# Performance work log

Measured on AMD Instinct MI355X. Metric: run time of the kernel, lower is better.

Reference implementation:

```python
import jax, jax.numpy as jnp
import numpy as np

N_NODES = 100000
D_IN = 128
D_OUT = 128
N_REL = 4
N_EDGES = 500000


def setup_inputs() -> dict:
    key = jax.random.key(0)
    k_x, k_e, k_w, k_b, k_ws, k_bs = jax.random.split(key, 6)
    x = jax.random.normal(k_x, (N_NODES, D_IN), dtype=jnp.float32)
    # edge_indices[r] = [2, E]: row 0 = source node ids, row 1 = target node ids
    edge_indices = jax.random.randint(k_e, (N_REL, 2, N_EDGES), 0, N_NODES, dtype=jnp.int32)
    scale = 1.0 / np.sqrt(D_IN)
    # per-relation Linear weights (out, in) and biases, like nn.Linear
    W = jax.random.uniform(k_w, (N_REL, D_OUT, D_IN), dtype=jnp.float32, minval=-scale, maxval=scale)
    b = jax.random.uniform(k_b, (N_REL, D_OUT), dtype=jnp.float32, minval=-scale, maxval=scale)
    W_sl = jax.random.uniform(k_ws, (D_OUT, D_IN), dtype=jnp.float32, minval=-scale, maxval=scale)
    b_sl = jax.random.uniform(k_bs, (D_OUT,), dtype=jnp.float32, minval=-scale, maxval=scale)
    return {"x": x, "edge_indices": edge_indices, "W": W, "b": b, "W_sl": W_sl, "b_sl": b_sl}


def reference(x, edge_indices, W, b, W_sl, b_sl):
    # gather source features per relation: [R, E, D_IN]
    src = edge_indices[:, 0]  # [R, E]
    tgt = edge_indices[:, 1]  # [R, E]
    xs = x[src]  # [R, E, D_IN]
    # per-relation linear (nn.Linear: x @ W.T + b): [R, E, D_OUT]
    msgs = jnp.einsum('red,rfd->ref', xs, W) + b[:, None, :]
    # scatter-add into per-relation node accumulators, then sum over relations
    agg = jax.vmap(lambda m, t: jax.ops.segment_sum(m, t, num_segments=N_NODES))(msgs, tgt)
    agg = agg.sum(axis=0)  # [N, D_OUT]
    # self loop
    agg = agg + x @ W_sl.T + b_sl
    return agg
```

## Files before the change

### kernel.cpp

```cpp
#include <hip/hip_runtime.h>
#include <hip/hip_bf16.h>

#define N_NODES 100000
#define D 128
#define N_REL 4
#define N_EDGES 500000
#define N_CNT (N_REL * N_NODES)
#define SCAN_CHUNK 1024
#define N_SCAN_BLK ((N_CNT + SCAN_CHUNK - 1) / SCAN_CHUNK)
#define SORT_MAX (N_REL * N_EDGES + 3 * N_CNT)

typedef __attribute__((ext_vector_type(8))) short bf16x8;
typedef __attribute__((ext_vector_type(4))) float f32x4;

__device__ __forceinline__ unsigned short f2bf(float f) {
    unsigned int u = __float_as_uint(f);
    u += 0x7fffu + ((u >> 16) & 1u);
    return (unsigned short)(u >> 16);
}

#define CVT_BLOCKS 6250
#define WB_BLOCKS 320
#define ZR_BLOCKS 1
#define HIST_BLOCKS 7813
__global__ __launch_bounds__(256) void prep_kernel(const float* __restrict__ x,
                                                   const int* __restrict__ ei,
                                                   const float* __restrict__ W,
                                                   const float* __restrict__ W_sl,
                                                   ushort* __restrict__ xbf,
                                                   ushort* __restrict__ WbT,
                                                   int* __restrict__ cnt) {
    const int b = blockIdx.x, tid = threadIdx.x;
    if (b < CVT_BLOCKS) {
        size_t t = (size_t)b * 256 + tid;
        float4 v0 = ((const float4*)x)[t * 2];
        float4 v1 = ((const float4*)x)[t * 2 + 1];
        int4 o;
        o.x = ((int)f2bf(v0.y) << 16) | f2bf(v0.x);
        o.y = ((int)f2bf(v0.w) << 16) | f2bf(v0.z);
        o.z = ((int)f2bf(v1.y) << 16) | f2bf(v1.x);
        o.w = ((int)f2bf(v1.w) << 16) | f2bf(v1.z);
        ((int4*)xbf)[t] = o;
    } else if (b < CVT_BLOCKS + WB_BLOCKS) {
        int t = (b - CVT_BLOCKS) * 256 + tid;
        int f = t / 640;
        int k = t - f * 640;
        float v;
        if (k < 512) {
            int r = k >> 7, d = k & 127;
            v = W[((size_t)r * 128 + f) * 128 + d];
        } else {
            v = W_sl[(size_t)f * 128 + (k - 512)];
        }
        WbT[t] = f2bf(v);
    } else if (b < CVT_BLOCKS + WB_BLOCKS + ZR_BLOCKS) {
        if (tid < 16) ((uint4*)(xbf + (size_t)N_NODES * D))[tid] = make_uint4(0, 0, 0, 0);
    } else {
        int t = (b - CVT_BLOCKS - WB_BLOCKS - ZR_BLOCKS) * 256 + tid;
        if (t >= N_REL * N_EDGES) return;
        int r = t / N_EDGES;
        int e = t - r * N_EDGES;
        int tgt = ei[(size_t)r * 2 * N_EDGES + N_EDGES + e];
        atomicAdd(&cnt[r * N_NODES + tgt], 1);
    }
}

__global__ __launch_bounds__(256) void scanA(const int* __restrict__ cnt,
                                             int* __restrict__ foff,
                                             int* __restrict__ partials) {
    __shared__ int ps[256];
    int b = blockIdx.x, t = threadIdx.x;
    int i0 = b * SCAN_CHUNK + t * 4;
    int v[4];
#pragma unroll
    for (int q = 0; q < 4; ++q) v[q] = (i0 + q < N_CNT) ? ((cnt[i0 + q] + 3) & ~3) : 0;
    int s = v[0] + v[1] + v[2] + v[3];
    ps[t] = s;
    __syncthreads();
    for (int d = 1; d < 256; d <<= 1) {
        int u = (t >= d) ? ps[t - d] : 0;
        __syncthreads();
        ps[t] += u;
        __syncthreads();
    }
    if (t == 255) partials[b] = ps[255];
    int run = (t == 0) ? 0 : ps[t - 1];
#pragma unroll
    for (int q = 0; q < 4; ++q) {
        if (i0 + q < N_CNT) foff[i0 + q] = run;
        run += v[q];
    }
}
__global__ __launch_bounds__(512) void scanB(int* __restrict__ partials,
                                             int* __restrict__ foff) {
    __shared__ int ps[512];
    int t = threadIdx.x;
    ps[t] = (t < N_SCAN_BLK) ? partials[t] : 0;
    __syncthreads();
    for (int d = 1; d < 512; d <<= 1) {
        int u = (t >= d) ? ps[t - d] : 0;
        __syncthreads();
        ps[t] += u;
        __syncthreads();
    }
    if (t < N_SCAN_BLK) partials[t] = (t == 0) ? 0 : ps[t - 1];
    if (t == N_SCAN_BLK - 1) foff[N_CNT] = ps[t];
}
__global__ __launch_bounds__(256) void scanC(int* __restrict__ foff,
                                             const int* __restrict__ partials,
                                             const int* __restrict__ cnt,
                                             int* __restrict__ cur0,
                                             int* __restrict__ sorted) {
    int i = blockIdx.x * 256 + threadIdx.x;
    if (i >= N_CNT) return;
    int base = foff[i] + partials[i >> 10];
    foff[i] = base;
    cur0[i] = 0;
    int c = cnt[i];
    int cp = (c + 3) & ~3;
    for (int j = c; j < cp; ++j) sorted[base + j] = N_NODES;
}

__global__ __launch_bounds__(256) void bucket_kernel(const int* __restrict__ ei,
                                                     const int* __restrict__ foff,
                                                     int* __restrict__ cur0,
                                                     int* __restrict__ sorted) {
    int t = blockIdx.x * 256 + threadIdx.x;
    if (t >= N_REL * N_EDGES) return;
    int r = t / N_EDGES;
    int e = t - r * N_EDGES;
    int src = ei[(size_t)r * 2 * N_EDGES + e];
    int tgt = ei[(size_t)r * 2 * N_EDGES + N_EDGES + e];
    int i = r * N_NODES + tgt;
    int pos = foff[i] + atomicAdd(&cur0[i], 1);
    sorted[pos] = src;
}

__global__ __launch_bounds__(256) void gather_kernel(const ushort* __restrict__ xbf,
                                                     const int* __restrict__ sorted,
                                                     const int* __restrict__ foff,
                                                     unsigned int* __restrict__ buf) {
    int wid = (blockIdx.x * 256 + threadIdx.x) >> 6;
    wid = __builtin_amdgcn_readfirstlane(wid);
    const int lane = threadIdx.x & 63;
    const int p0 = wid * 4;
    int f0 = foff[p0], f1 = foff[p0 + 1], f2 = foff[p0 + 2], f3 = foff[p0 + 3], f4 = foff[p0 + 4];
#pragma unroll
    for (int pi = 0; pi < 4; ++pi) {
        int gb = (pi == 0) ? f0 : (pi == 1) ? f1 : (pi == 2) ? f2 : f3;
        int ge = (pi == 0) ? f1 : (pi == 1) ? f2 : (pi == 2) ? f3 : f4;
        float ax = 0.f, ay = 0.f;
        for (int g = gb; g < ge; g += 4) {
            int4 s = *(const int4*)(sorted + g);
            unsigned int u0 = ((const unsigned int*)(xbf + ((size_t)s.x << 7)))[lane];
            unsigned int u1 = ((const unsigned int*)(xbf + ((size_t)s.y << 7)))[lane];
            unsigned int u2 = ((const unsigned int*)(xbf + ((size_t)s.z << 7)))[lane];
            unsigned int u3 = ((const unsigned int*)(xbf + ((size_t)s.w << 7)))[lane];
            ax += __uint_as_float(u0 << 16) + __uint_as_float(u1 << 16)
                + __uint_as_float(u2 << 16) + __uint_as_float(u3 << 16);
            ay += __uint_as_float(u0 & 0xffff0000u) + __uint_as_float(u1 & 0xffff0000u)
                + __uint_as_float(u2 & 0xffff0000u) + __uint_as_float(u3 & 0xffff0000u);
        }
        buf[(size_t)(p0 + pi) * 64 + lane] = ((unsigned int)f2bf(ay) << 16) | f2bf(ax);
    }
}

__global__ __launch_bounds__(256) void gemm_kernel(const ushort* __restrict__ buf,
                                                   const ushort* __restrict__ xbf,
                                                   const ushort* __restrict__ WbT,
                                                   const int* __restrict__ cnt,
                                                   const float* __restrict__ bias,
                                                   const float* __restrict__ b_sl,
                                                   float* __restrict__ out) {
    __shared__ __align__(16) ushort As[128 * 72];
    __shared__ __align__(16) ushort Bs[128 * 72];
    __shared__ float degS[4 * 128];
    __shared__ float biasS[4 * 128];
    __shared__ float bslS[128];

    const int tid = threadIdx.x;
    const int l = tid & 63, w = tid >> 6;
    const int wr = w >> 1, wc = w & 1;
    const int lr = l & 15, lq = l >> 4;
    const int n0 = blockIdx.x * 128;

#pragma unroll
    for (int it = 0; it < 2; ++it) {
        int idx = it * 256 + tid;
        int r = idx >> 7, row = idx & 127;
        int n = n0 + row;
        degS[idx] = (n < N_NODES) ? (float)cnt[r * N_NODES + n] : 0.f;
        biasS[idx] = bias[idx];
    }
    if (tid < 128) bslS[tid] = b_sl[tid];

    f32x4 acc[4][4];
#pragma unroll
    for (int mi = 0; mi < 4; ++mi)
#pragma unroll
        for (int ni = 0; ni < 4; ++ni) acc[mi][ni] = (f32x4){0.f, 0.f, 0.f, 0.f};

    const int ar_ = (tid * 4) >> 3 >> 0;
    int4 aReg[4], bReg[4];

    auto LOAD = [&](int kt) {
        const int region = kt >> 1;
        const int d0 = (kt & 1) * 64;
#pragma unroll
        for (int it = 0; it < 4; ++it) {
            int id = it * 256 + tid;
            int r_ = id >> 3, c16 = id & 7;
            int n = n0 + r_;
            if (n > N_NODES - 1) n = N_NODES - 1;
            const ushort* sp = (region < 4)
                ? ((const ushort*)buf + (((size_t)region * N_NODES + n) << 7) + d0)
                : (xbf + ((size_t)n << 7) + d0);
            aReg[it] = *(const int4*)(sp + c16 * 8);
        }
#pragma unroll
        for (int it = 0; it < 4; ++it) {
            int id = it * 256 + tid;
            int f_ = id >> 3, c16 = id & 7;
            bReg[it] = *(const int4*)(WbT + (size_t)f_ * 640 + kt * 64 + c16 * 8);
        }
    };

    LOAD(0);
    for (int kt = 0; kt < 10; ++kt) {
        __syncthreads();
#pragma unroll
        for (int it = 0; it < 4; ++it) {
            int id = it * 256 + tid;
            int r_ = id >> 3, c16 = id & 7;
            *(int4*)(As + r_ * 72 + c16 * 8) = aReg[it];
            *(int4*)(Bs + r_ * 72 + c16 * 8) = bReg[it];
        }
        __syncthreads();
        if (kt < 9) LOAD(kt + 1);
#pragma unroll
        for (int ks = 0; ks < 2; ++ks) {
            bf16x8 a[4], bb[4];
#pragma unroll
            for (int mi = 0; mi < 4; ++mi)
                a[mi] = *(const bf16x8*)(As + (wr * 64 + mi * 16 + lr) * 72 + ks * 32 + lq * 8);
#pragma unroll
            for (int ni = 0; ni < 4; ++ni)
                bb[ni] = *(const bf16x8*)(Bs + (wc * 64 + ni * 16 + lr) * 72 + ks * 32 + lq * 8);
#pragma unroll
            for (int mi = 0; mi < 4; ++mi)
#pragma unroll
                for (int ni = 0; ni < 4; ++ni)
                    acc[mi][ni] = __builtin_amdgcn_mfma_f32_16x16x32_bf16(a[mi], bb[ni], acc[mi][ni], 0, 0, 0);
        }
    }

    float bw[4][4], bsl_[4];
#pragma unroll
    for (int ni = 0; ni < 4; ++ni) {
        int f = wc * 64 + ni * 16 + lr;
        bsl_[ni] = bslS[f];
#pragma unroll
        for (int r = 0; r < 4; ++r) bw[ni][r] = biasS[r * 128 + f];
    }
#pragma unroll
    for (int mi = 0; mi < 4; ++mi) {
#pragma unroll
        for (int q = 0; q < 4; ++q) {
            int row = wr * 64 + mi * 16 + lq * 4 + q;
            int n = n0 + row;
            if (n >= N_NODES) continue;
            float d0_ = degS[row], d1_ = degS[128 + row], d2_ = degS[256 + row], d3_ = degS[384 + row];
#pragma unroll
            for (int ni = 0; ni < 4; ++ni) {
                int f = wc * 64 + ni * 16 + lr;
                float v = acc[mi][ni][q] + d0_ * bw[ni][0] + d1_ * bw[ni][1]
                        + d2_ * bw[ni][2] + d3_ * bw[ni][3] + bsl_[ni];
                out[(size_t)n * 128 + f] = v;
            }
        }
    }
}

extern "C" void kernel_launch(void* const* d_in, const int* in_sizes, int n_in,
                              void* d_out, int out_size, void* d_ws, size_t ws_size,
                              hipStream_t stream) {
    const float* x    = (const float*)d_in[0];
    const int*   ei   = (const int*)d_in[1];
    const float* W    = (const float*)d_in[2];
    const float* b    = (const float*)d_in[3];
    const float* W_sl = (const float*)d_in[4];
    const float* b_sl = (const float*)d_in[5];
    float* out = (float*)d_out;

    int*          cnt      = (int*)d_ws;
    int*          cur0     = cnt + N_CNT;
    int*          foff     = cur0 + N_CNT;
    int*          partials = foff + N_CNT + 64;
    ushort*       WbT      = (ushort*)(partials + 512);
    ushort*       xbf      = WbT + 128 * 640;
    int*          sorted   = (int*)(xbf + (size_t)(N_NODES + 1) * D + 64);
    unsigned int* buf      = (unsigned int*)(sorted + SORT_MAX);

    hipMemsetAsync(cnt, 0, N_CNT * sizeof(int), stream);

    prep_kernel<<<CVT_BLOCKS + WB_BLOCKS + ZR_BLOCKS + HIST_BLOCKS, 256, 0, stream>>>(
        x, ei, W, W_sl, xbf, WbT, cnt);
    scanA<<<N_SCAN_BLK, 256, 0, stream>>>(cnt, foff, partials);
    scanB<<<1, 512, 0, stream>>>(partials, foff);
    scanC<<<(N_CNT + 255) / 256, 256, 0, stream>>>(foff, partials, cnt, cur0, sorted);
    bucket_kernel<<<(N_REL * N_EDGES + 255) / 256, 256, 0, stream>>>(ei, foff, cur0, sorted);
    gather_kernel<<<N_CNT / 16, 256, 0, stream>>>(xbf, sorted, foff, buf);
    gemm_kernel<<<(N_NODES + 127) / 128, 256, 0, stream>>>((const ushort*)buf, xbf, WbT, cnt, b, b_sl, out);
}
```

Measured before the change: 483.3 us.

## Drop scanB launch, swizzle GEMM LDS tiles, stage output through LDS for coalesced stores

The single-block scanB kernel is removed, and each scanC block now reduces the scanA partials that precede it to get its offset, which saves one launch at the cost of redundant reads. The GEMM replaces padded LDS tiles with XOR-swizzled unpadded tiles and drops the register prefetch of the next K tile, so loads are no longer overlapped with MFMA. The epilogue writes accumulators into LDS and then stores coalesced float4 rows instead of scattered scalar stores. The buf pointer expression also drops a cast, which may not compile if buf keeps its unsigned int type.

```diff
diff --git a/kernel.cpp b/kernel.cpp
--- a/kernel.cpp
+++ b/kernel.cpp
@@ -91,34 +91,33 @@
         run += v[q];
     }
 }
-__global__ __launch_bounds__(512) void scanB(int* __restrict__ partials,
-                                             int* __restrict__ foff) {
-    __shared__ int ps[512];
-    int t = threadIdx.x;
-    ps[t] = (t < N_SCAN_BLK) ? partials[t] : 0;
-    __syncthreads();
-    for (int d = 1; d < 512; d <<= 1) {
-        int u = (t >= d) ? ps[t - d] : 0;
-        __syncthreads();
-        ps[t] += u;
-        __syncthreads();
-    }
-    if (t < N_SCAN_BLK) partials[t] = (t == 0) ? 0 : ps[t - 1];
-    if (t == N_SCAN_BLK - 1) foff[N_CNT] = ps[t];
-}
+
 __global__ __launch_bounds__(256) void scanC(int* __restrict__ foff,
                                              const int* __restrict__ partials,
                                              const int* __restrict__ cnt,
                                              int* __restrict__ cur0,
                                              int* __restrict__ sorted) {
-    int i = blockIdx.x * 256 + threadIdx.x;
+    __shared__ int red[256];
+    const int b = blockIdx.x, t = threadIdx.x;
+    const int pb = b >> 2;
+    int s = 0;
+    for (int j = t; j < pb; j += 256) s += partials[j];
+    red[t] = s;
+    __syncthreads();
+    for (int d = 128; d > 0; d >>= 1) {
+        if (t < d) red[t] += red[t + d];
+        __syncthreads();
+    }
+    const int P = red[0];
+    int i = b * 256 + t;
     if (i >= N_CNT) return;
-    int base = foff[i] + partials[i >> 10];
+    int base = foff[i] + P;
     foff[i] = base;
     cur0[i] = 0;
     int c = cnt[i];
     int cp = (c + 3) & ~3;
     for (int j = c; j < cp; ++j) sorted[base + j] = N_NODES;
+    if (i == N_CNT - 1) foff[N_CNT] = base + cp;
 }
 
 __global__ __launch_bounds__(256) void bucket_kernel(const int* __restrict__ ei,
@@ -172,11 +171,12 @@
                                                    const float* __restrict__ bias,
                                                    const float* __restrict__ b_sl,
                                                    float* __restrict__ out) {
-    __shared__ __align__(16) ushort As[128 * 72];
-    __shared__ __align__(16) ushort Bs[128 * 72];
+    __shared__ __align__(16) float SH[64 * 132];
     __shared__ float degS[4 * 128];
     __shared__ float biasS[4 * 128];
     __shared__ float bslS[128];
+    ushort* As = (ushort*)SH;
+    ushort* Bs = As + 128 * 64;
 
     const int tid = threadIdx.x;
     const int l = tid & 63, w = tid >> 6;
@@ -200,10 +200,8 @@
 #pragma unroll
         for (int ni = 0; ni < 4; ++ni) acc[mi][ni] = (f32x4){0.f, 0.f, 0.f, 0.f};
 
-    const int ar_ = (tid * 4) >> 3 >> 0;
-    int4 aReg[4], bReg[4];
-
-    auto LOAD = [&](int kt) {
+    for (int kt = 0; kt < 10; ++kt) {
+        __syncthreads();
         const int region = kt >> 1;
         const int d0 = (kt & 1) * 64;
 #pragma unroll
@@ -213,39 +211,25 @@
             int n = n0 + r_;
             if (n > N_NODES - 1) n = N_NODES - 1;
             const ushort* sp = (region < 4)
-                ? ((const ushort*)buf + (((size_t)region * N_NODES + n) << 7) + d0)
+                ? (buf + (((size_t)region * N_NODES + n) << 7) + d0)
                 : (xbf + ((size_t)n << 7) + d0);
-            aReg[it] = *(const int4*)(sp + c16 * 8);
-        }
-#pragma unroll
-        for (int it = 0; it < 4; ++it) {
-            int id = it * 256 + tid;
-            int f_ = id >> 3, c16 = id & 7;
-            bReg[it] = *(const int4*)(WbT + (size_t)f_ * 640 + kt * 64 + c16 * 8);
-        }
-    };
-
-    LOAD(0);
-    for (int kt = 0; kt < 10; ++kt) {
-        __syncthreads();
-#pragma unroll
-        for (int it = 0; it < 4; ++it) {
-            int id = it * 256 + tid;
-            int r_ = id >> 3, c16 = id & 7;
-            *(int4*)(As + r_ * 72 + c16 * 8) = aReg[it];
-            *(int4*)(Bs + r_ * 72 + c16 * 8) = bReg[it];
-        }
-        __syncthreads();
-        if (kt < 9) LOAD(kt + 1);
+            int4 va = *(const int4*)(sp + c16 * 8);
+            *(int4*)(As + r_ * 64 + ((c16 ^ (r_ & 7)) << 3)) = va;
+            int4 vb = *(const int4*)(WbT + (size_t)r_ * 640 + kt * 64 + c16 * 8);
+            *(int4*)(Bs + r_ * 64 + ((c16 ^ (r_ & 7)) << 3)) = vb;
+        }
+        __syncthreads();
 #pragma unroll
         for (int ks = 0; ks < 2; ++ks) {
+            const int ch = ks * 4 + lq;
+            const int chs = (ch ^ (lr & 7)) << 3;
             bf16x8 a[4], bb[4];
 #pragma unroll
             for (int mi = 0; mi < 4; ++mi)
-                a[mi] = *(const bf16x8*)(As + (wr * 64 + mi * 16 + lr) * 72 + ks * 32 + lq * 8);
+                a[mi] = *(const bf16x8*)(As + (wr * 64 + mi * 16 + lr) * 64 + chs);
 #pragma unroll
             for (int ni = 0; ni < 4; ++ni)
-                bb[ni] = *(const bf16x8*)(Bs + (wc * 64 + ni * 16 + lr) * 72 + ks * 32 + lq * 8);
+                bb[ni] = *(const bf16x8*)(Bs + (wc * 64 + ni * 16 + lr) * 64 + chs);
 #pragma unroll
             for (int mi = 0; mi < 4; ++mi)
 #pragma unroll
@@ -262,21 +246,34 @@
 #pragma unroll
         for (int r = 0; r < 4; ++r) bw[ni][r] = biasS[r * 128 + f];
     }
-#pragma unroll
-    for (int mi = 0; mi < 4; ++mi) {
-#pragma unroll
-        for (int q = 0; q < 4; ++q) {
-            int row = wr * 64 + mi * 16 + lq * 4 + q;
-            int n = n0 + row;
-            if (n >= N_NODES) continue;
-            float d0_ = degS[row], d1_ = degS[128 + row], d2_ = degS[256 + row], d3_ = degS[384 + row];
-#pragma unroll
-            for (int ni = 0; ni < 4; ++ni) {
-                int f = wc * 64 + ni * 16 + lr;
-                float v = acc[mi][ni][q] + d0_ * bw[ni][0] + d1_ * bw[ni][1]
-                        + d2_ * bw[ni][2] + d3_ * bw[ni][3] + bsl_[ni];
-                out[(size_t)n * 128 + f] = v;
-            }
+    float* Cs = SH;
+#pragma unroll
+    for (int h = 0; h < 2; ++h) {
+        __syncthreads();
+        if (wr == h) {
+#pragma unroll
+            for (int mi = 0; mi < 4; ++mi)
+#pragma unroll
+                for (int q = 0; q < 4; ++q) {
+                    int row = mi * 16 + lq * 4 + q;
+                    int gr = h * 64 + row;
+                    float d0_ = degS[gr], d1_ = degS[128 + gr], d2_ = degS[256 + gr], d3_ = degS[384 + gr];
+#pragma unroll
+                    for (int ni = 0; ni < 4; ++ni) {
+                        int f = wc * 64 + ni * 16 + lr;
+                        Cs[row * 132 + f] = acc[mi][ni][q] + d0_ * bw[ni][0] + d1_ * bw[ni][1]
+                                          + d2_ * bw[ni][2] + d3_ * bw[ni][3] + bsl_[ni];
+                    }
+                }
+        }
+        __syncthreads();
+#pragma unroll
+        for (int it = 0; it < 8; ++it) {
+            int idx = it * 256 + tid;
+            int row = idx >> 5, c4 = idx & 31;
+            int n = n0 + h * 64 + row;
+            if (n < N_NODES)
+                *(float4*)(out + (size_t)n * 128 + c4 * 4) = *(const float4*)(Cs + row * 132 + c4 * 4);
         }
     }
 }
@@ -306,7 +303,6 @@
     prep_kernel<<<CVT_BLOCKS + WB_BLOCKS + ZR_BLOCKS + HIST_BLOCKS, 256, 0, stream>>>(
         x, ei, W, W_sl, xbf, WbT, cnt);
     scanA<<<N_SCAN_BLK, 256, 0, stream>>>(cnt, foff, partials);
-    scanB<<<1, 512, 0, stream>>>(partials, foff);
     scanC<<<(N_CNT + 255) / 256, 256, 0, stream>>>(foff, partials, cnt, cur0, sorted);
     bucket_kernel<<<(N_REL * N_EDGES + 255) / 256, 256, 0, stream>>>(ei, foff, cur0, sorted);
     gather_kernel<<<N_CNT / 16, 256, 0, stream>>>(xbf, sorted, foff, buf);
```

Result: faster. 415.2 us (-14.1%).
